# Performance work log

Hardware: AMD Instinct MI355X
Metric: run time of the kernel (lower is better)

The kernel has to match this reference:

```python
import jax, jax.numpy as jnp
import numpy as np

B, T, C = 4, 2048, 1024
H = 16
D = C // H  # head_dim = 64


def setup_inputs() -> dict:
    key = jax.random.key(0)
    ks = jax.random.split(key, 5)
    scale_in = 1.0 / np.sqrt(C)
    x = jax.random.normal(ks[0], (B, T, C), dtype=jnp.float32)
    w_qkv = jax.random.normal(ks[1], (C, 3 * C), dtype=jnp.float32) * scale_in
    b_qkv = jnp.zeros((3 * C,), dtype=jnp.float32)
    w_proj = jax.random.normal(ks[2], (C, C), dtype=jnp.float32) * scale_in
    b_proj = jnp.zeros((C,), dtype=jnp.float32)
    return {"x": x, "w_qkv": w_qkv, "b_qkv": b_qkv, "w_proj": w_proj, "b_proj": b_proj}


def reference(x, w_qkv, b_qkv, w_proj, b_proj):
    # fused QKV projection: [B,T,3C]
    qkv = x @ w_qkv + b_qkv
    q, k, v = jnp.split(qkv, 3, axis=-1)
    # [B,T,C] -> [B,H,T,D]
    q = q.reshape(B, T, H, D).transpose(0, 2, 1, 3)
    k = k.reshape(B, T, H, D).transpose(0, 2, 1, 3)
    v = v.reshape(B, T, H, D).transpose(0, 2, 1, 3)
    scale = 1.0 / np.sqrt(D)
    scores = jnp.einsum('bhqd,bhkd->bhqk', q, k) * scale  # [B,H,T,T]
    causal = jnp.tril(jnp.ones((T, T), dtype=bool))
    scores = jnp.where(causal, scores, jnp.finfo(scores.dtype).min)
    attn = jax.nn.softmax(scores, axis=-1)
    y = jnp.einsum('bhqk,bhkd->bhqd', attn, v)  # [B,H,T,D]
    y = y.transpose(0, 2, 1, 3).reshape(B, T, C)
    return y @ w_proj + b_proj
```

## Files before the change

kernel.cpp:

```cpp
#include <hip/hip_runtime.h>

typedef unsigned short u16;
typedef unsigned int u32;
typedef unsigned long long u64;
typedef __attribute__((ext_vector_type(8))) short s16x8;
typedef __attribute__((ext_vector_type(4))) float f32x4;

#if __has_builtin(__builtin_amdgcn_exp2f)
#define EXP2(x) __builtin_amdgcn_exp2f(x)
#else
#define EXP2(x) __expf((x) * 0.69314718f)
#endif

#if __has_builtin(__builtin_amdgcn_rcpf)
#define RCP(x) __builtin_amdgcn_rcpf(x)
#else
#define RCP(x) (1.0f / (x))
#endif

#define GLL(gp, lp) __builtin_amdgcn_global_load_lds(                         \
    (const __attribute__((address_space(1))) unsigned int*)(const void*)(gp), \
    (__attribute__((address_space(3))) unsigned int*)(void*)(lp), 16, 0, 0)

__device__ __forceinline__ u16 f2bf(float f) {
    union { float f; u32 u; } v; v.f = f;
    u32 r = v.u + 0x7FFF + ((v.u >> 16) & 1);
    return (u16)(r >> 16);
}

__device__ __forceinline__ u16 f2bf_trunc(float f) {
    union { float f; u32 u; } v; v.f = f;
    return (u16)(v.u >> 16);
}

__device__ __forceinline__ float bf2f(u16 b) {
    union { u32 u; float f; } v; v.u = ((u32)b) << 16;
    return v.f;
}

__device__ __forceinline__ s16x8 scale_frag(s16x8 v, float s) {
    s16x8 o;
#pragma unroll
    for (int i = 0; i < 8; i++) o[i] = (short)f2bf(bf2f((u16)v[i]) * s);
    return o;
}

__global__ __launch_bounds__(256) void cast_f32_bf16(const float* __restrict__ in,
                                                     u16* __restrict__ out) {
    size_t i = ((size_t)blockIdx.x * 256 + threadIdx.x) * 4;
    float4 f = *(const float4*)(in + i);
    u16 o[4] = { f2bf(f.x), f2bf(f.y), f2bf(f.z), f2bf(f.w) };
    *(unsigned long long*)(out + i) =
        (unsigned long long)o[0] | ((unsigned long long)o[1] << 16) |
        ((unsigned long long)o[2] << 32) | ((unsigned long long)o[3] << 48);
}

__global__ __launch_bounds__(256) void transpose_cast(const float* __restrict__ in,
                                                      u16* __restrict__ out,
                                                      int rows, int cols) {
    __shared__ float tile[32][33];
    int c0 = blockIdx.x * 32, r0 = blockIdx.y * 32;
    int tx = threadIdx.x, ty = threadIdx.y;
    for (int i = 0; i < 32; i += 8)
        tile[ty + i][tx] = in[(size_t)(r0 + ty + i) * cols + (c0 + tx)];
    __syncthreads();
    for (int i = 0; i < 32; i += 8)
        out[(size_t)(c0 + ty + i) * rows + (r0 + tx)] = f2bf(tile[tx][ty + i]);
}

template<int MODE>
__global__ __launch_bounds__(256, 4) void gemm_bt64(const u16* __restrict__ A,
                                                    const u16* __restrict__ BT,
                                                    const float* __restrict__ bias,
                                                    void* __restrict__ O1,
                                                    u16* __restrict__ vT,
                                                    int M, int N, int K) {
    __shared__ u16 SMEM[18432];
    u16* As = SMEM;
    u16* Bs = SMEM + 8192;
    int n0 = blockIdx.x * 128, m0 = blockIdx.y * 128;
    int tid = threadIdx.x, lane = tid & 63, w = tid >> 6;
    int row16 = lane & 15, quad = lane >> 4;
    int wm = (w >> 1) * 64, wn = (w & 1) * 64;
    f32x4 acc[4][4] = {};

    int lr = lane >> 3;
    int cswz = (lane & 7) ^ lr;
    const u16* Ag = A + (size_t)(m0 + w * 32 + lr) * K + cswz * 8;
    const u16* Bg = BT + (size_t)(n0 + w * 32 + lr) * K + cswz * 8;
    u16* Asl = As + (w * 32) * 64;
    u16* Bsl = Bs + (w * 32) * 64;

    for (int k0 = 0; k0 < K; k0 += 64) {
        __syncthreads();
#pragma unroll
        for (int j = 0; j < 4; j++) {
            GLL(Ag + k0 + (size_t)j * 8 * K, Asl + j * 8 * 64);
            GLL(Bg + k0 + (size_t)j * 8 * K, Bsl + j * 8 * 64);
        }
        __syncthreads();
#pragma unroll
        for (int kk = 0; kk < 2; kk++) {
            s16x8 af[4], bf[4];
#pragma unroll
            for (int mi = 0; mi < 4; mi++)
                af[mi] = *(const s16x8*)&As[(wm + mi * 16 + row16) * 64 +
                                            (((kk * 4 + quad) ^ (row16 & 7)) * 8)];
#pragma unroll
            for (int ni = 0; ni < 4; ni++)
                bf[ni] = *(const s16x8*)&Bs[(wn + ni * 16 + row16) * 64 +
                                            (((kk * 4 + quad) ^ (row16 & 7)) * 8)];
#pragma unroll
            for (int mi = 0; mi < 4; mi++)
#pragma unroll
                for (int ni = 0; ni < 4; ni++)
                    acc[mi][ni] = __builtin_amdgcn_mfma_f32_16x16x32_bf16(
                        af[mi], bf[ni], acc[mi][ni], 0, 0, 0);
        }
    }

    if (MODE == 0) {
        float* O = (float*)O1;
#pragma unroll
        for (int ni = 0; ni < 4; ni++) {
            int col = n0 + wn + ni * 16 + row16;
            float bv = bias[col];
#pragma unroll
            for (int mi = 0; mi < 4; mi++)
#pragma unroll
                for (int r = 0; r < 4; r++)
                    O[(size_t)(m0 + wm + mi * 16 + quad * 4 + r) * N + col] =
                        acc[mi][ni][r] + bv;
        }
    } else if (n0 < 2048) {
        u16* qk = (u16*)O1;
#pragma unroll
        for (int ni = 0; ni < 4; ni++) {
            int col = n0 + wn + ni * 16 + row16;
            float bv = bias[col];
#pragma unroll
            for (int mi = 0; mi < 4; mi++)
#pragma unroll
                for (int r = 0; r < 4; r++)
                    qk[(size_t)(m0 + wm + mi * 16 + quad * 4 + r) * 2048 + col] =
                        f2bf(acc[mi][ni][r] + bv);
        }
    } else {
        __syncthreads();
        u16* scr = SMEM + w * 64 * 72;
#pragma unroll
        for (int ni = 0; ni < 4; ni++) {
            float bv = bias[n0 + wn + ni * 16 + row16];
#pragma unroll
            for (int mi = 0; mi < 4; mi++)
#pragma unroll
                for (int r = 0; r < 4; r++)
                    scr[(ni * 16 + row16) * 72 + (mi * 16 + quad * 4 + r)] =
                        f2bf(acc[mi][ni][r] + bv);
        }
        __syncthreads();
        int r8 = lane >> 3, c8 = lane & 7;
        int vbase = (m0 >> 11) * 1024 + (n0 - 2048) + wn;
        int tb = (m0 & 2047) + wm;
#pragma unroll
        for (int it = 0; it < 8; it++) {
            s16x8 vv = *(const s16x8*)&scr[(it * 8 + r8) * 72 + c8 * 8];
            *(s16x8*)&vT[(size_t)(vbase + it * 8 + r8) * 2048 + tb + c8 * 8] = vv;
        }
    }
}

__global__ __launch_bounds__(256, 4) void attn_kernel(const u16* __restrict__ qk,
                                                      const u16* __restrict__ vT,
                                                      u16* __restrict__ y) {
    __shared__ u16 Kb[2][64 * 64];
    __shared__ u16 Vb[2][64 * 64];
    __shared__ u16 Ps[4 * 16 * 64];

    int tid = threadIdx.x, lane = tid & 63, w = tid >> 6;
    int row16 = lane & 15, quad = lane >> 4;
    int id = blockIdx.x;
    int xcd = id & 7, slot = id >> 3;
    int pairi = slot >> 3;
    int bh = ((slot & 7) << 3) | xcd;
    int b = bh >> 4, h = bh & 15;
    const u16* qkb = qk + (size_t)b * 2048 * 2048;
    const u16* vtb = vT + ((size_t)(b * 1024) + h * 64) * 2048;

    int lr = lane >> 3, cswz = (lane & 7) ^ lr;
    const u16* Kg = qkb + (size_t)(w * 16 + lr) * 2048 + 1024 + h * 64 + cswz * 8;
    const u16* Vg = vtb + (size_t)(w * 16 + lr) * 2048 + cswz * 8;
    u16* Psw = Ps + w * 1024;
    int sw = row16 & 7;

    s16x8 ones;
#pragma unroll
    for (int i = 0; i < 8; i++) ones[i] = (short)0x3F80;
    const float qs = 0.125f * 1.44269504f;

    for (int half = 0; half < 2; half++) {
        int qt = half ? pairi : (31 - pairi);
        int q0 = qt * 64;
        int niter = qt + 1;

        int qrow = q0 + w * 16 + row16;
        const u16* qp = qkb + (size_t)qrow * 2048 + h * 64 + quad * 8;
        s16x8 qf0 = scale_frag(*(const s16x8*)qp, qs);
        s16x8 qf1 = scale_frag(*(const s16x8*)(qp + 32), qs);

        f32x4 acc_o[4] = {};
        f32x4 acc_l = {};

        __syncthreads();
#pragma unroll
        for (int j = 0; j < 2; j++) {
            GLL(Kg + (size_t)j * 8 * 2048, Kb[0] + w * 16 * 64 + j * 8 * 64);
            GLL(Vg + (size_t)j * 8 * 2048, Vb[0] + w * 16 * 64 + j * 8 * 64);
        }

        for (int kb = 0; kb < niter; kb++) {
            int cur = kb & 1;
            __syncthreads();
            if (kb + 1 < niter) {
                int k1 = (kb + 1) * 64;
#pragma unroll
                for (int j = 0; j < 2; j++) {
                    GLL(Kg + (size_t)(k1 + j * 8) * 2048, Kb[cur ^ 1] + w * 16 * 64 + j * 8 * 64);
                    GLL(Vg + k1 + (size_t)j * 8 * 2048, Vb[cur ^ 1] + w * 16 * 64 + j * 8 * 64);
                }
            }
            const u16* Kc = Kb[cur];
            const u16* Vc = Vb[cur];
            int k0 = kb * 64;

            f32x4 s[4];
#pragma unroll
            for (int nk = 0; nk < 4; nk++) {
                s16x8 kf0 = *(const s16x8*)&Kc[(nk * 16 + row16) * 64 + ((quad ^ sw) * 8)];
                s16x8 kf1 = *(const s16x8*)&Kc[(nk * 16 + row16) * 64 + (((4 + quad) ^ sw) * 8)];
                f32x4 z = {};
                z = __builtin_amdgcn_mfma_f32_16x16x32_bf16(qf0, kf0, z, 0, 0, 0);
                z = __builtin_amdgcn_mfma_f32_16x16x32_bf16(qf1, kf1, z, 0, 0, 0);
                s[nk] = z;
            }
            if (kb == niter - 1) {
                int rowb = q0 + w * 16 + quad * 4;
#pragma unroll
                for (int nk = 0; nk < 4; nk++) {
                    int kj = k0 + nk * 16 + row16;
#pragma unroll
                    for (int r = 0; r < 4; r++)
                        if (kj > rowb + r) s[nk][r] = -__builtin_inff();
                }
            }
#pragma unroll
            for (int nk = 0; nk < 4; nk++)
#pragma unroll
                for (int r = 0; r < 4; r++) {
                    float p = EXP2(s[nk][r]);
                    int qr = quad * 4 + r;
                    Psw[qr * 64 + (((nk * 2 + (row16 >> 3)) ^ (qr & 7)) * 8) + (row16 & 7)] =
                        f2bf_trunc(p);
                }
#pragma unroll
            for (int kk = 0; kk < 2; kk++) {
                s16x8 pf = *(const s16x8*)&Psw[row16 * 64 + (((kk * 4 + quad) ^ sw) * 8)];
#pragma unroll
                for (int nd = 0; nd < 4; nd++) {
                    s16x8 vf = *(const s16x8*)&Vc[(nd * 16 + row16) * 64 +
                                                  (((kk * 4 + quad) ^ sw) * 8)];
                    acc_o[nd] = __builtin_amdgcn_mfma_f32_16x16x32_bf16(pf, vf, acc_o[nd], 0, 0, 0);
                }
                acc_l = __builtin_amdgcn_mfma_f32_16x16x32_bf16(pf, ones, acc_l, 0, 0, 0);
            }
        }

        int t0 = q0 + w * 16 + quad * 4;
#pragma unroll
        for (int r = 0; r < 4; r++) {
            float inv = RCP(acc_l[r]);
#pragma unroll
            for (int nd = 0; nd < 4; nd++)
                y[((size_t)b * 2048 + t0 + r) * 1024 + h * 64 + nd * 16 + row16] =
                    f2bf(acc_o[nd][r] * inv);
        }
    }
}

extern "C" void kernel_launch(void* const* d_in, const int* in_sizes, int n_in,
                              void* d_out, int out_size, void* d_ws, size_t ws_size,
                              hipStream_t stream) {
    const float* x      = (const float*)d_in[0];
    const float* w_qkv  = (const float*)d_in[1];
    const float* b_qkv  = (const float*)d_in[2];
    const float* w_proj = (const float*)d_in[3];
    const float* b_proj = (const float*)d_in[4];
    float* out = (float*)d_out;

    u16* ws     = (u16*)d_ws;
    u16* x_bf   = ws;
    u16* wqkvT  = x_bf  + (size_t)8192 * 1024;
    u16* wprojT = wqkvT + (size_t)3072 * 1024;
    u16* qkbuf  = wprojT + (size_t)1024 * 1024;
    u16* vT     = qkbuf + (size_t)8192 * 2048;
    u16* ybf    = vT    + (size_t)4096 * 2048;

    cast_f32_bf16<<<dim3(8192), dim3(256), 0, stream>>>(x, x_bf);
    transpose_cast<<<dim3(96, 32), dim3(32, 8), 0, stream>>>(w_qkv, wqkvT, 1024, 3072);
    transpose_cast<<<dim3(32, 32), dim3(32, 8), 0, stream>>>(w_proj, wprojT, 1024, 1024);
    gemm_bt64<1><<<dim3(24, 64), 256, 0, stream>>>(x_bf, wqkvT, b_qkv, (void*)qkbuf, vT, 8192, 3072, 1024);
    attn_kernel<<<dim3(1024), 256, 0, stream>>>(qkbuf, vT, ybf);
    gemm_bt64<0><<<dim3(8, 64), 256, 0, stream>>>(ybf, wprojT, b_proj, (void*)out, nullptr, 8192, 1024, 1024);
}
```

Measured before the change: 233.5 us.

## Enlarge attention query tile to 128 rows and remap GEMM blocks per XCD

```diff
diff --git a/kernel.cpp b/kernel.cpp
--- a/kernel.cpp
+++ b/kernel.cpp
@@ -28,9 +28,9 @@
     return (u16)(r >> 16);
 }
 
-__device__ __forceinline__ u16 f2bf_trunc(float f) {
-    union { float f; u32 u; } v; v.f = f;
-    return (u16)(v.u >> 16);
+__device__ __forceinline__ u32 pack2_trunc(float a, float b) {
+    union { float f; u32 u; } x, y; x.f = a; y.f = b;
+    return (x.u >> 16) | (y.u & 0xFFFF0000u);
 }
 
 __device__ __forceinline__ float bf2f(u16 b) {
@@ -68,7 +68,7 @@
         out[(size_t)(c0 + ty + i) * rows + (r0 + tx)] = f2bf(tile[tx][ty + i]);
 }
 
-template<int MODE>
+template<int MODE, int NB>
 __global__ __launch_bounds__(256, 4) void gemm_bt64(const u16* __restrict__ A,
                                                     const u16* __restrict__ BT,
                                                     const float* __restrict__ bias,
@@ -78,7 +78,10 @@
     __shared__ u16 SMEM[18432];
     u16* As = SMEM;
     u16* Bs = SMEM + 8192;
-    int n0 = blockIdx.x * 128, m0 = blockIdx.y * 128;
+    int id = blockIdx.x;
+    int xcd = id & 7, s = id >> 3;
+    int ni = s % NB, mi8 = s / NB;
+    int n0 = ni * 128, m0 = (xcd * 8 + mi8) * 128;
     int tid = threadIdx.x, lane = tid & 63, w = tid >> 6;
     int row16 = lane & 15, quad = lane >> 4;
     int wm = (w >> 1) * 64, wn = (w & 1) * 64;
@@ -107,56 +110,56 @@
                 af[mi] = *(const s16x8*)&As[(wm + mi * 16 + row16) * 64 +
                                             (((kk * 4 + quad) ^ (row16 & 7)) * 8)];
 #pragma unroll
-            for (int ni = 0; ni < 4; ni++)
-                bf[ni] = *(const s16x8*)&Bs[(wn + ni * 16 + row16) * 64 +
-                                            (((kk * 4 + quad) ^ (row16 & 7)) * 8)];
-#pragma unroll
-            for (int mi = 0; mi < 4; mi++)
-#pragma unroll
-                for (int ni = 0; ni < 4; ni++)
-                    acc[mi][ni] = __builtin_amdgcn_mfma_f32_16x16x32_bf16(
-                        af[mi], bf[ni], acc[mi][ni], 0, 0, 0);
+            for (int ni2 = 0; ni2 < 4; ni2++)
+                bf[ni2] = *(const s16x8*)&Bs[(wn + ni2 * 16 + row16) * 64 +
+                                             (((kk * 4 + quad) ^ (row16 & 7)) * 8)];
+#pragma unroll
+            for (int mi = 0; mi < 4; mi++)
+#pragma unroll
+                for (int ni2 = 0; ni2 < 4; ni2++)
+                    acc[mi][ni2] = __builtin_amdgcn_mfma_f32_16x16x32_bf16(
+                        af[mi], bf[ni2], acc[mi][ni2], 0, 0, 0);
         }
     }
 
     if (MODE == 0) {
         float* O = (float*)O1;
 #pragma unroll
-        for (int ni = 0; ni < 4; ni++) {
-            int col = n0 + wn + ni * 16 + row16;
+        for (int ni2 = 0; ni2 < 4; ni2++) {
+            int col = n0 + wn + ni2 * 16 + row16;
             float bv = bias[col];
 #pragma unroll
             for (int mi = 0; mi < 4; mi++)
 #pragma unroll
                 for (int r = 0; r < 4; r++)
                     O[(size_t)(m0 + wm + mi * 16 + quad * 4 + r) * N + col] =
-                        acc[mi][ni][r] + bv;
+                        acc[mi][ni2][r] + bv;
         }
     } else if (n0 < 2048) {
         u16* qk = (u16*)O1;
 #pragma unroll
-        for (int ni = 0; ni < 4; ni++) {
-            int col = n0 + wn + ni * 16 + row16;
+        for (int ni2 = 0; ni2 < 4; ni2++) {
+            int col = n0 + wn + ni2 * 16 + row16;
             float bv = bias[col];
 #pragma unroll
             for (int mi = 0; mi < 4; mi++)
 #pragma unroll
                 for (int r = 0; r < 4; r++)
                     qk[(size_t)(m0 + wm + mi * 16 + quad * 4 + r) * 2048 + col] =
-                        f2bf(acc[mi][ni][r] + bv);
+                        f2bf(acc[mi][ni2][r] + bv);
         }
     } else {
         __syncthreads();
         u16* scr = SMEM + w * 64 * 72;
 #pragma unroll
-        for (int ni = 0; ni < 4; ni++) {
-            float bv = bias[n0 + wn + ni * 16 + row16];
+        for (int ni2 = 0; ni2 < 4; ni2++) {
+            float bv = bias[n0 + wn + ni2 * 16 + row16];
 #pragma unroll
             for (int mi = 0; mi < 4; mi++)
 #pragma unroll
                 for (int r = 0; r < 4; r++)
-                    scr[(ni * 16 + row16) * 72 + (mi * 16 + quad * 4 + r)] =
-                        f2bf(acc[mi][ni][r] + bv);
+                    scr[(ni2 * 16 + row16) * 72 + (mi * 16 + quad * 4 + r)] =
+                        f2bf(acc[mi][ni2][r] + bv);
         }
         __syncthreads();
         int r8 = lane >> 3, c8 = lane & 7;
@@ -170,12 +173,12 @@
     }
 }
 
-__global__ __launch_bounds__(256, 4) void attn_kernel(const u16* __restrict__ qk,
+__global__ __launch_bounds__(256, 2) void attn_kernel(const u16* __restrict__ qk,
                                                       const u16* __restrict__ vT,
                                                       u16* __restrict__ y) {
-    __shared__ u16 Kb[2][64 * 64];
-    __shared__ u16 Vb[2][64 * 64];
-    __shared__ u16 Ps[4 * 16 * 64];
+    __shared__ u16 Kb[2][4096];
+    __shared__ u16 Vb[2][4096];
+    __shared__ u16 Ps[4][2048];
 
     int tid = threadIdx.x, lane = tid & 63, w = tid >> 6;
     int row16 = lane & 15, quad = lane >> 4;
@@ -190,7 +193,7 @@
     int lr = lane >> 3, cswz = (lane & 7) ^ lr;
     const u16* Kg = qkb + (size_t)(w * 16 + lr) * 2048 + 1024 + h * 64 + cswz * 8;
     const u16* Vg = vtb + (size_t)(w * 16 + lr) * 2048 + cswz * 8;
-    u16* Psw = Ps + w * 1024;
+    u16* Psw = Ps[w];
     int sw = row16 & 7;
 
     s16x8 ones;
@@ -199,17 +202,21 @@
     const float qs = 0.125f * 1.44269504f;
 
     for (int half = 0; half < 2; half++) {
-        int qt = half ? pairi : (31 - pairi);
-        int q0 = qt * 64;
-        int niter = qt + 1;
-
-        int qrow = q0 + w * 16 + row16;
-        const u16* qp = qkb + (size_t)qrow * 2048 + h * 64 + quad * 8;
-        s16x8 qf0 = scale_frag(*(const s16x8*)qp, qs);
-        s16x8 qf1 = scale_frag(*(const s16x8*)(qp + 32), qs);
-
-        f32x4 acc_o[4] = {};
-        f32x4 acc_l = {};
+        int qt = half ? pairi : (15 - pairi);
+        int q0 = qt * 128;
+        int niter = 2 * qt + 2;
+        int qw = q0 + w * 32;
+
+        s16x8 qf[2][2];
+#pragma unroll
+        for (int mi = 0; mi < 2; mi++) {
+            const u16* qp = qkb + (size_t)(qw + mi * 16 + row16) * 2048 + h * 64 + quad * 8;
+            qf[mi][0] = scale_frag(*(const s16x8*)qp, qs);
+            qf[mi][1] = scale_frag(*(const s16x8*)(qp + 32), qs);
+        }
+
+        f32x4 acc_o[2][4] = {};
+        f32x4 acc_l[2] = {};
 
         __syncthreads();
 #pragma unroll
@@ -229,60 +236,78 @@
                     GLL(Vg + k1 + (size_t)j * 8 * 2048, Vb[cur ^ 1] + w * 16 * 64 + j * 8 * 64);
                 }
             }
+            int k0 = kb * 64;
+            if (k0 > qw + 31) continue;
             const u16* Kc = Kb[cur];
             const u16* Vc = Vb[cur];
-            int k0 = kb * 64;
-
-            f32x4 s[4];
+
+            f32x4 sc[2][4];
 #pragma unroll
             for (int nk = 0; nk < 4; nk++) {
                 s16x8 kf0 = *(const s16x8*)&Kc[(nk * 16 + row16) * 64 + ((quad ^ sw) * 8)];
                 s16x8 kf1 = *(const s16x8*)&Kc[(nk * 16 + row16) * 64 + (((4 + quad) ^ sw) * 8)];
-                f32x4 z = {};
-                z = __builtin_amdgcn_mfma_f32_16x16x32_bf16(qf0, kf0, z, 0, 0, 0);
-                z = __builtin_amdgcn_mfma_f32_16x16x32_bf16(qf1, kf1, z, 0, 0, 0);
-                s[nk] = z;
-            }
-            if (kb == niter - 1) {
-                int rowb = q0 + w * 16 + quad * 4;
+#pragma unroll
+                for (int mi = 0; mi < 2; mi++) {
+                    f32x4 z = {};
+                    z = __builtin_amdgcn_mfma_f32_16x16x32_bf16(kf0, qf[mi][0], z, 0, 0, 0);
+                    z = __builtin_amdgcn_mfma_f32_16x16x32_bf16(kf1, qf[mi][1], z, 0, 0, 0);
+                    sc[mi][nk] = z;
+                }
+            }
+            if (k0 + 63 > qw) {
+#pragma unroll
+                for (int mi = 0; mi < 2; mi++) {
+                    int qg = qw + mi * 16 + row16;
+#pragma unroll
+                    for (int nk = 0; nk < 4; nk++) {
+                        int kbase = k0 + nk * 16 + quad * 4;
+#pragma unroll
+                        for (int r = 0; r < 4; r++)
+                            if (kbase + r > qg) sc[mi][nk][r] = -__builtin_inff();
+                    }
+                }
+            }
+#pragma unroll
+            for (int mi = 0; mi < 2; mi++)
 #pragma unroll
                 for (int nk = 0; nk < 4; nk++) {
-                    int kj = k0 + nk * 16 + row16;
-#pragma unroll
-                    for (int r = 0; r < 4; r++)
-                        if (kj > rowb + r) s[nk][r] = -__builtin_inff();
-                }
-            }
-#pragma unroll
-            for (int nk = 0; nk < 4; nk++)
-#pragma unroll
-                for (int r = 0; r < 4; r++) {
-                    float p = EXP2(s[nk][r]);
-                    int qr = quad * 4 + r;
-                    Psw[qr * 64 + (((nk * 2 + (row16 >> 3)) ^ (qr & 7)) * 8) + (row16 & 7)] =
-                        f2bf_trunc(p);
+                    float p0 = EXP2(sc[mi][nk][0]);
+                    float p1 = EXP2(sc[mi][nk][1]);
+                    float p2 = EXP2(sc[mi][nk][2]);
+                    float p3 = EXP2(sc[mi][nk][3]);
+                    u32 w0 = pack2_trunc(p0, p1);
+                    u32 w1 = pack2_trunc(p2, p3);
+                    int u = nk * 2 + (quad >> 1);
+                    int eo = ((u ^ sw) * 8) + (quad & 1) * 4;
+                    *(u64*)&Psw[mi * 1024 + row16 * 64 + eo] = (u64)w0 | ((u64)w1 << 32);
                 }
 #pragma unroll
             for (int kk = 0; kk < 2; kk++) {
-                s16x8 pf = *(const s16x8*)&Psw[row16 * 64 + (((kk * 4 + quad) ^ sw) * 8)];
+                int co = ((kk * 4 + quad) ^ sw) * 8;
+                s16x8 pf0 = *(const s16x8*)&Psw[row16 * 64 + co];
+                s16x8 pf1 = *(const s16x8*)&Psw[1024 + row16 * 64 + co];
 #pragma unroll
                 for (int nd = 0; nd < 4; nd++) {
-                    s16x8 vf = *(const s16x8*)&Vc[(nd * 16 + row16) * 64 +
-                                                  (((kk * 4 + quad) ^ sw) * 8)];
-                    acc_o[nd] = __builtin_amdgcn_mfma_f32_16x16x32_bf16(pf, vf, acc_o[nd], 0, 0, 0);
-                }
-                acc_l = __builtin_amdgcn_mfma_f32_16x16x32_bf16(pf, ones, acc_l, 0, 0, 0);
-            }
-        }
-
-        int t0 = q0 + w * 16 + quad * 4;
-#pragma unroll
-        for (int r = 0; r < 4; r++) {
-            float inv = RCP(acc_l[r]);
-#pragma unroll
-            for (int nd = 0; nd < 4; nd++)
-                y[((size_t)b * 2048 + t0 + r) * 1024 + h * 64 + nd * 16 + row16] =
-                    f2bf(acc_o[nd][r] * inv);
+                    s16x8 vf = *(const s16x8*)&Vc[(nd * 16 + row16) * 64 + co];
+                    acc_o[0][nd] = __builtin_amdgcn_mfma_f32_16x16x32_bf16(pf0, vf, acc_o[0][nd], 0, 0, 0);
+                    acc_o[1][nd] = __builtin_amdgcn_mfma_f32_16x16x32_bf16(pf1, vf, acc_o[1][nd], 0, 0, 0);
+                }
+                acc_l[0] = __builtin_amdgcn_mfma_f32_16x16x32_bf16(pf0, ones, acc_l[0], 0, 0, 0);
+                acc_l[1] = __builtin_amdgcn_mfma_f32_16x16x32_bf16(pf1, ones, acc_l[1], 0, 0, 0);
+            }
+        }
+
+#pragma unroll
+        for (int mi = 0; mi < 2; mi++) {
+            int t0 = qw + mi * 16 + quad * 4;
+#pragma unroll
+            for (int r = 0; r < 4; r++) {
+                float inv = RCP(acc_l[mi][r]);
+#pragma unroll
+                for (int nd = 0; nd < 4; nd++)
+                    y[((size_t)b * 2048 + t0 + r) * 1024 + h * 64 + nd * 16 + row16] =
+                        f2bf(acc_o[mi][nd][r] * inv);
+            }
         }
     }
 }
@@ -308,7 +333,7 @@
     cast_f32_bf16<<<dim3(8192), dim3(256), 0, stream>>>(x, x_bf);
     transpose_cast<<<dim3(96, 32), dim3(32, 8), 0, stream>>>(w_qkv, wqkvT, 1024, 3072);
     transpose_cast<<<dim3(32, 32), dim3(32, 8), 0, stream>>>(w_proj, wprojT, 1024, 1024);
-    gemm_bt64<1><<<dim3(24, 64), 256, 0, stream>>>(x_bf, wqkvT, b_qkv, (void*)qkbuf, vT, 8192, 3072, 1024);
-    attn_kernel<<<dim3(1024), 256, 0, stream>>>(qkbuf, vT, ybf);
-    gemm_bt64<0><<<dim3(8, 64), 256, 0, stream>>>(ybf, wprojT, b_proj, (void*)out, nullptr, 8192, 1024, 1024);
-}
+    gemm_bt64<1, 24><<<dim3(1536), 256, 0, stream>>>(x_bf, wqkvT, b_qkv, (void*)qkbuf, vT, 8192, 3072, 1024);
+    attn_kernel<<<dim3(512), 256, 0, stream>>>(qkbuf, vT, ybf);
+    gemm_bt64<0, 8><<<dim3(512), 256, 0, stream>>>(ybf, wprojT, b_proj, (void*)out, nullptr, 8192, 1024, 1024);
+}
```

Result: no change. 230.7 us (-1.2%).
